# Optimization experiments

Measured on AMD Instinct MI355X. Metric: run time of the kernel, lower is better.

## Reference

```python
import jax, jax.numpy as jnp
import numpy as np

S, B = 1000, 64
E, P, D, O = 512, 256, 1024, 128  # embedding_dim, prenet_dim, decoder_dim, output_dim


def setup_inputs() -> dict:
    key = jax.random.key(0)
    ks = jax.random.split(key, 12)
    u = lambda k, shape: jax.random.uniform(k, shape, jnp.float32, -0.1, 0.1)
    return {
        "encoder_out": jax.random.normal(ks[0], (S, B, E), jnp.float32),
        "mels": jax.random.normal(ks[1], (S, B, O), jnp.float32),
        # prenet layer 0: Linear(O -> P), layer 1: Linear(P -> P)
        "pre_W1": u(ks[2], (P, O)), "pre_b1": u(ks[3], (P,)),
        "pre_W2": u(ks[4], (P, P)), "pre_b2": u(ks[5], (P,)),
        # LSTMCell(input=P+E, hidden=D); gate order i,f,g,o
        "W_ih": u(ks[6], (4 * D, P + E)), "W_hh": u(ks[7], (4 * D, D)),
        "b_ih": u(ks[8], (4 * D,)), "b_hh": u(ks[9], (4 * D,)),
        # projection: Linear(D+E -> O)
        "proj_W": u(ks[10], (O, D + E)), "proj_b": u(ks[11], (O,)),
    }


def reference(encoder_out, mels, pre_W1, pre_b1, pre_W2, pre_b2,
              W_ih, W_hh, b_ih, b_hh, proj_W, proj_b):
    # Teacher forcing: prepend <GO> zero frame, drop last mel frame (only S inputs used)
    go = jnp.zeros((1, B, O), encoder_out.dtype)
    dec_in = jnp.concatenate([go, mels[:-1]], axis=0)  # [S, B, O]
    # Prenet (dropout in eval mode => identity), vectorized over all frames
    x = jax.nn.relu(jnp.einsum('sbo,po->sbp', dec_in, pre_W1) + pre_b1)
    x = jax.nn.relu(jnp.einsum('sbp,qp->sbq', x, pre_W2) + pre_b2)  # [S, B, P]
    # Pre-compute input-to-hidden gate contributions for every frame (big GEMM once)
    lstm_in = jnp.concatenate([x, encoder_out], axis=-1)  # [S, B, P+E]
    gates_x = jnp.einsum('sbi,gi->sbg', lstm_in, W_ih) + b_ih + b_hh  # [S, B, 4D]

    def step(carry, gx_t):
        h, c = carry
        gates = gx_t + h @ W_hh.T  # [B, 4D]
        i, f, g, o = jnp.split(gates, 4, axis=-1)
        c_new = jax.nn.sigmoid(f) * c + jax.nn.sigmoid(i) * jnp.tanh(g)
        h_new = jax.nn.sigmoid(o) * jnp.tanh(c_new)
        # zoneout=0.0 -> new state kept exactly
        return (h_new, c_new), h_new

    h0 = jnp.zeros((B, D), encoder_out.dtype)
    c0 = jnp.zeros((B, D), encoder_out.dtype)
    _, hs = jax.lax.scan(step, (h0, c0), gates_x)  # hs: [S, B, D]

    out = jnp.concatenate([hs, encoder_out], axis=-1)  # [S, B, D+E]
    return jnp.einsum('sbd,od->sbo', out, proj_W) + proj_b  # [S, B, O]
```

## Files before the change

kernel.cpp:

```cpp
#include <hip/hip_runtime.h>
#include <stdint.h>

typedef __bf16 bf16x8 __attribute__((ext_vector_type(8)));
typedef float f32x4 __attribute__((ext_vector_type(4)));
typedef unsigned short ushort_t;

__device__ __forceinline__ float b2f(ushort_t u) {
  union { unsigned int i; float f; } x; x.i = ((unsigned int)u) << 16; return x.f;
}
__device__ __forceinline__ ushort_t f2b(float f) {
  union { float f; unsigned int i; } x; x.f = f;
  unsigned int r = x.i + 0x7fffu + ((x.i >> 16) & 1u);
  return (ushort_t)(r >> 16);
}
__device__ __forceinline__ float b2f_elem(ushort4 v, int j) {
  const ushort_t u = (j == 0) ? v.x : (j == 1) ? v.y : (j == 2) ? v.z : v.w;
  return b2f(u);
}
__device__ __forceinline__ float ftanh(float x) {
  const float e2 = __expf(2.f * x);
  return 1.f - 2.f / (e2 + 1.f);
}

__global__ __launch_bounds__(256) void cvt_f32_bf16(const float* __restrict__ src,
                                                    ushort_t* __restrict__ dst,
                                                    int n4)
{
  const int i = blockIdx.x * 256 + threadIdx.x;
  if (i >= n4) return;
  const float4 v = ((const float4*)src)[i];
  ushort4 o;
  o.x = f2b(v.x); o.y = f2b(v.y); o.z = f2b(v.z); o.w = f2b(v.w);
  ((ushort4*)dst)[i] = o;
}

__global__ __launch_bounds__(256) void build_decin(const float* __restrict__ mels,
                                                   ushort_t* __restrict__ dec,
                                                   int t0, int n4)
{
  const int i = blockIdx.x * 256 + threadIdx.x;
  if (i >= n4) return;
  const int gr = t0 * 64 + (i >> 5);
  ushort4 o;
  if (gr < 64) {
    o.x = o.y = o.z = o.w = 0;
  } else {
    const float4 v = ((const float4*)mels)[(size_t)(gr - 64) * 32 + (i & 31)];
    o.x = f2b(v.x); o.y = f2b(v.y); o.z = f2b(v.z); o.w = f2b(v.w);
  }
  ((ushort4*)dec)[i] = o;
}

__global__ __launch_bounds__(256) void gemm_bt(
    const ushort_t* __restrict__ A1, int lda1, int K1,
    const ushort_t* __restrict__ A2, int lda2, int K2,
    const ushort_t* __restrict__ B,
    const float* __restrict__ bias1, const float* __restrict__ bias2,
    void* __restrict__ C, int ldc, int relu, int out_f32)
{
  __shared__ __align__(16) ushort_t As[128 * 72];
  __shared__ __align__(16) ushort_t Bs[128 * 72];
  const int tid = threadIdx.x;
  const int wave = tid >> 6, lane = tid & 63;
  const int bm = blockIdx.x, bn = blockIdx.y;
  const int wm = (wave & 1) * 64, wn = (wave >> 1) * 64;
  const int l15 = lane & 15, quad = lane >> 4;
  const int ldb = K1 + K2;

  f32x4 acc[4][4] = {};

  const int kb1 = K1 >> 6, kb2 = K2 >> 6;
  for (int kb = 0; kb < kb1 + kb2; ++kb) {
    const bool ph2 = (kb >= kb1);
    const ushort_t* Aptr = ph2 ? A2 : A1;
    const int lda = ph2 ? lda2 : lda1;
    const int k0 = ph2 ? ((kb - kb1) << 6) : (kb << 6);
    const int bk0 = ph2 ? (K1 + k0) : k0;

#pragma unroll
    for (int s = 0; s < 4; ++s) {
      const int ch = s * 256 + tid;
      const int row = ch >> 3, pos = ch & 7;
      const bf16x8 av = *(const bf16x8*)(Aptr + (size_t)(bm * 128 + row) * lda
                                         + k0 + pos * 8);
      *(bf16x8*)(As + row * 72 + pos * 8) = av;
      const bf16x8 bv = *(const bf16x8*)(B + (size_t)(bn * 128 + row) * ldb
                                         + bk0 + pos * 8);
      *(bf16x8*)(Bs + row * 72 + pos * 8) = bv;
    }
    __syncthreads();

#pragma unroll
    for (int ks = 0; ks < 2; ++ks) {
      bf16x8 af[4], bfr[4];
      const int c = ks * 4 + quad;
#pragma unroll
      for (int mt = 0; mt < 4; ++mt)
        af[mt] = *(const bf16x8*)(As + (wm + mt * 16 + l15) * 72 + c * 8);
#pragma unroll
      for (int nt = 0; nt < 4; ++nt)
        bfr[nt] = *(const bf16x8*)(Bs + (wn + nt * 16 + l15) * 72 + c * 8);
#pragma unroll
      for (int mt = 0; mt < 4; ++mt)
#pragma unroll
        for (int nt = 0; nt < 4; ++nt)
          acc[mt][nt] = __builtin_amdgcn_mfma_f32_16x16x32_bf16(
              af[mt], bfr[nt], acc[mt][nt], 0, 0, 0);
    }
    __syncthreads();
  }

#pragma unroll
  for (int nt = 0; nt < 4; ++nt) {
    const int n = bn * 128 + wn + nt * 16 + l15;
    float bsum = 0.f;
    if (bias1) bsum += bias1[n];
    if (bias2) bsum += bias2[n];
#pragma unroll
    for (int mt = 0; mt < 4; ++mt) {
#pragma unroll
      for (int r = 0; r < 4; ++r) {
        const int m = bm * 128 + wm + mt * 16 + quad * 4 + r;
        float v = acc[mt][nt][r] + bsum;
        if (relu) v = fmaxf(v, 0.f);
        if (out_f32) ((float*)C)[(size_t)m * ldc + n] = v;
        else         ((ushort_t*)C)[(size_t)m * ldc + n] = f2b(v);
      }
    }
  }
}

__global__ __launch_bounds__(256, 1) void lstm_persist(
    const ushort_t* __restrict__ gates,
    const ushort_t* __restrict__ Whh,
    ushort_t* __restrict__ hs,
    float* __restrict__ cst,
    int T, int* __restrict__ flags,
    int expect)
{
  __shared__ float red[4][2][64][17];
  const int tid = threadIdx.x;
  const int g = tid >> 6, lane = tid & 63;
  const int l15 = lane & 15, quad = lane >> 4;
  const int nb = blockIdx.x;
  const int ds = nb * 16;

  bf16x8 warr[4][8];
#pragma unroll
  for (int gg = 0; gg < 4; ++gg) {
    const ushort_t* wrow =
        Whh + (size_t)(gg * 1024 + ds + l15) * 1024 + g * 256 + quad * 8;
#pragma unroll
    for (int ks = 0; ks < 8; ++ks)
      warr[gg][ks] = *(const bf16x8*)(wrow + ks * 32);
  }

  const int eb = tid >> 2, edl = (tid & 3) * 4;
  f32x4 creg = *(const f32x4*)(cst + eb * 1024 + ds + edl);

  for (int s = 0; s < T; ++s) {
    const ushort_t* gx_t =
        gates + (size_t)s * 262144 + (size_t)eb * 4096 + ds + edl;
    const ushort4 gxv0 = *(const ushort4*)(gx_t);
    const ushort4 gxv1 = *(const ushort4*)(gx_t + 1024);
    const ushort4 gxv2 = *(const ushort4*)(gx_t + 2048);
    const ushort4 gxv3 = *(const ushort4*)(gx_t + 3072);
    asm volatile("" ::: "memory");

    if (s > 0) {
      int* fp = flags + (s - 1) * 64 + lane;
      int v = __hip_atomic_load(fp, __ATOMIC_RELAXED, __HIP_MEMORY_SCOPE_AGENT);
      while (!__all(v == expect)) {
        __builtin_amdgcn_s_sleep(1);
        v = __hip_atomic_load(fp, __ATOMIC_RELAXED, __HIP_MEMORY_SCOPE_AGENT);
      }
      asm volatile("" ::: "memory");
    }

    const ushort_t* hb =
        hs + (size_t)s * 65536 + l15 * 1024 + g * 256 + quad * 8;
    f32x4 acc[4][4] = {};
#pragma unroll
    for (int ks = 0; ks < 8; ++ks) {
      bf16x8 a[4];
#pragma unroll
      for (int mt = 0; mt < 4; ++mt)
        a[mt] = *(const bf16x8*)(hb + mt * 16384 + ks * 32);
#pragma unroll
      for (int gg = 0; gg < 4; ++gg)
#pragma unroll
        for (int mt = 0; mt < 4; ++mt)
          acc[gg][mt] = __builtin_amdgcn_mfma_f32_16x16x32_bf16(
              a[mt], warr[gg][ks], acc[gg][mt], 0, 0, 0);
    }

    float gf4[4][4];
#pragma unroll
    for (int rnd = 0; rnd < 2; ++rnd) {
#pragma unroll
      for (int ggl = 0; ggl < 2; ++ggl) {
        const int gg = rnd * 2 + ggl;
#pragma unroll
        for (int mt = 0; mt < 4; ++mt)
#pragma unroll
          for (int r = 0; r < 4; ++r)
            red[g][ggl][mt * 16 + quad * 4 + r][l15] = acc[gg][mt][r];
      }
      __syncthreads();
#pragma unroll
      for (int ggl = 0; ggl < 2; ++ggl)
#pragma unroll
        for (int j = 0; j < 4; ++j)
          gf4[rnd * 2 + ggl][j] =
              red[0][ggl][eb][edl + j] + red[1][ggl][eb][edl + j] +
              red[2][ggl][eb][edl + j] + red[3][ggl][eb][edl + j];
      if (rnd == 0) __syncthreads();
    }

    ushort_t* hdst = hs + (size_t)(s + 1) * 65536 + eb * 1024 + ds + edl;
    union { ushort_t u[4]; unsigned long long ll; } pk;
#pragma unroll
    for (int j = 0; j < 4; ++j) {
      const float gi = gf4[0][j] + b2f_elem(gxv0, j);
      const float gf = gf4[1][j] + b2f_elem(gxv1, j);
      const float gc = gf4[2][j] + b2f_elem(gxv2, j);
      const float go = gf4[3][j] + b2f_elem(gxv3, j);
      const float si = 1.f / (1.f + __expf(-gi));
      const float sf = 1.f / (1.f + __expf(-gf));
      const float so = 1.f / (1.f + __expf(-go));
      const float cn = sf * creg[j] + si * ftanh(gc);
      creg[j] = cn;
      pk.u[j] = f2b(so * ftanh(cn));
    }
    __hip_atomic_store((unsigned long long*)hdst, pk.ll,
                       __ATOMIC_RELAXED, __HIP_MEMORY_SCOPE_AGENT);

    __syncthreads();
    if (tid == 0)
      __hip_atomic_store(flags + s * 64 + nb, expect,
                         __ATOMIC_RELAXED, __HIP_MEMORY_SCOPE_AGENT);
  }

  *(f32x4*)(cst + eb * 1024 + ds + edl) = creg;
}

extern "C" void kernel_launch(void* const* d_in, const int* in_sizes, int n_in,
                              void* d_out, int out_size, void* d_ws, size_t ws_size,
                              hipStream_t stream) {
  const float* enc   = (const float*)d_in[0];
  const float* mels  = (const float*)d_in[1];
  const float* preW1 = (const float*)d_in[2];
  const float* preb1 = (const float*)d_in[3];
  const float* preW2 = (const float*)d_in[4];
  const float* preb2 = (const float*)d_in[5];
  const float* Wih   = (const float*)d_in[6];
  const float* Whh   = (const float*)d_in[7];
  const float* bih   = (const float*)d_in[8];
  const float* bhh   = (const float*)d_in[9];
  const float* projW = (const float*)d_in[10];
  const float* projb = (const float*)d_in[11];
  float* out = (float*)d_out;

  const size_t fixedB = 32768 * 2 + 65536 * 2 + 3145728 * 2 + 4194304 * 2
                      + 196608 * 2 + 262144 + 51456 + 65536;
  const int cand[5] = {200, 100, 50, 10, 2};
  int T = 2;
  for (int ci = 0; ci < 5; ++ci) {
    const int t = cand[ci];
    size_t need = fixedB
                + (size_t)t * 524288
                + (size_t)t * 16384
                + (size_t)t * 65536
                + (size_t)t * 32768 * 2
                + (size_t)(t + 1) * 131072;
    if (need <= ws_size) { T = t; break; }
  }

  char* ws = (char*)d_ws;
  size_t off = 0;
  auto carve = [&](size_t bytes) {
    char* p = ws + off;
    off += (bytes + 255) & ~(size_t)255;
    return p;
  };
  ushort_t* wW1  = (ushort_t*)carve(32768 * 2);
  ushort_t* wW2  = (ushort_t*)carve(65536 * 2);
  ushort_t* wIh  = (ushort_t*)carve(3145728 * 2);
  ushort_t* wHh  = (ushort_t*)carve(4194304 * 2);
  ushort_t* wPj  = (ushort_t*)carve(196608 * 2);
  float*    cst  = (float*)carve(262144);
  int*      flags = (int*)carve(51200);
  ushort_t* gates = (ushort_t*)carve((size_t)T * 524288);
  ushort_t* decin = (ushort_t*)carve((size_t)T * 16384);
  ushort_t* enc_c = (ushort_t*)carve((size_t)T * 65536);
  ushort_t* x1    = (ushort_t*)carve((size_t)T * 32768);
  ushort_t* x2    = (ushort_t*)carve((size_t)T * 32768);
  ushort_t* hs    = (ushort_t*)carve((size_t)(T + 1) * 131072);

  cvt_f32_bf16<<<32, 256, 0, stream>>>(preW1, wW1, 8192);
  cvt_f32_bf16<<<64, 256, 0, stream>>>(preW2, wW2, 16384);
  cvt_f32_bf16<<<3072, 256, 0, stream>>>(Wih, wIh, 786432);
  cvt_f32_bf16<<<4096, 256, 0, stream>>>(Whh, wHh, 1048576);
  cvt_f32_bf16<<<192, 256, 0, stream>>>(projW, wPj, 49152);

  hipMemsetAsync(hs, 0, 131072, stream);
  hipMemsetAsync(cst, 0, 262144, stream);
  hipMemsetAsync(flags, 0, 51200, stream);

  const int nch = 1000 / T;
  const int Mb = (T * 64) / 128;

  for (int c = 0; c < nch; ++c) {
    const int t0 = c * T;

    cvt_f32_bf16<<<(T * 8192 + 255) / 256, 256, 0, stream>>>(
        enc + (size_t)t0 * 32768, enc_c, T * 8192);
    build_decin<<<T * 8, 256, 0, stream>>>(mels, decin, t0, T * 2048);

    gemm_bt<<<dim3(Mb, 2), 256, 0, stream>>>(decin, 128, 128, nullptr, 0, 0,
                                             wW1, preb1, nullptr, x1, 256, 1, 0);
    gemm_bt<<<dim3(Mb, 2), 256, 0, stream>>>(x1, 256, 256, nullptr, 0, 0,
                                             wW2, preb2, nullptr, x2, 256, 1, 0);
    gemm_bt<<<dim3(Mb, 32), 256, 0, stream>>>(x2, 256, 256, enc_c, 512, 512,
                                              wIh, bih, bhh, gates, 4096, 0, 0);
    lstm_persist<<<64, 256, 0, stream>>>(gates, wHh, hs, cst, T, flags, c + 1);

    gemm_bt<<<dim3(Mb, 1), 256, 0, stream>>>(hs + 65536, 1024, 1024, enc_c,
                                             512, 512, wPj, projb, nullptr,
                                             out + (size_t)t0 * 8192, 128, 0, 1);
    if (c + 1 < nch) {
      hipMemcpyAsync(hs, hs + (size_t)T * 65536, 131072,
                     hipMemcpyDeviceToDevice, stream);
    }
  }
}
```

Baseline: 8.337 ms.

## Stage h via global_load_lds into swizzled LDS and use per-wave flags

Each wave now copies its K-slice of the previous hidden state from global memory into a swizzled LDS buffer using direct global-to-LDS loads, then reads the MFMA A operands from LDS instead of issuing scattered global loads. Step completion flags go from one per block to one per wave, so a wave waits only on the 64 producer waves that wrote the K-slice it reads, not on whole blocks, and the block-wide barrier before signalling is removed. This aims to shorten the per-step latency of the serial recurrence. In exchange it adds a larger LDS footprint, an extra barrier, a fourfold larger flag array, and more flag polling traffic.

```diff
diff --git a/kernel.cpp b/kernel.cpp
--- a/kernel.cpp
+++ b/kernel.cpp
@@ -138,7 +138,10 @@
     int T, int* __restrict__ flags,
     int expect)
 {
-  __shared__ float red[4][2][64][17];
+  __shared__ __align__(16) ushort_t hq[4 * 64 * 256];
+  float* red = (float*)hq;
+#define RED(w, ggl, row, col) red[(((w) * 2 + (ggl)) * 64 + (row)) * 17 + (col)]
+
   const int tid = threadIdx.x;
   const int g = tid >> 6, lane = tid & 63;
   const int l15 = lane & 15, quad = lane >> 4;
@@ -157,6 +160,11 @@
 
   const int eb = tid >> 2, edl = (tid & 3) * 4;
   f32x4 creg = *(const f32x4*)(cst + eb * 1024 + ds + edl);
+
+  const int l5 = lane >> 5;
+  const int gc = lane & 31;
+  const int sx = l15 & 7;
+  ushort_t* hqg = hq + g * 16384;
 
   for (int s = 0; s < T; ++s) {
     const ushort_t* gx_t =
@@ -168,7 +176,7 @@
     asm volatile("" ::: "memory");
 
     if (s > 0) {
-      int* fp = flags + (s - 1) * 64 + lane;
+      int* fp = flags + (s - 1) * 256 + g * 64 + lane;
       int v = __hip_atomic_load(fp, __ATOMIC_RELAXED, __HIP_MEMORY_SCOPE_AGENT);
       while (!__all(v == expect)) {
         __builtin_amdgcn_s_sleep(1);
@@ -177,15 +185,29 @@
       asm volatile("" ::: "memory");
     }
 
-    const ushort_t* hb =
-        hs + (size_t)s * 65536 + l15 * 1024 + g * 256 + quad * 8;
+    {
+      const ushort_t* hsrc = hs + (size_t)s * 65536;
+#pragma unroll
+      for (int i = 0; i < 32; ++i) {
+        const int row = 2 * i + l5;
+        const int sg = gc ^ (row & 7);
+        const ushort_t* ga = hsrc + (size_t)row * 1024 + g * 256 + sg * 8;
+        __builtin_amdgcn_global_load_lds(
+            (const __attribute__((address_space(1))) void*)ga,
+            (__attribute__((address_space(3))) void*)(hqg + i * 512),
+            16, 0, 0);
+      }
+    }
+    asm volatile("s_waitcnt vmcnt(0)" ::: "memory");
+
     f32x4 acc[4][4] = {};
 #pragma unroll
     for (int ks = 0; ks < 8; ++ks) {
+      const int c = ks * 4 + quad;
       bf16x8 a[4];
 #pragma unroll
       for (int mt = 0; mt < 4; ++mt)
-        a[mt] = *(const bf16x8*)(hb + mt * 16384 + ks * 32);
+        a[mt] = *(const bf16x8*)(hqg + (mt * 16 + l15) * 256 + (c ^ sx) * 8);
 #pragma unroll
       for (int gg = 0; gg < 4; ++gg)
 #pragma unroll
@@ -193,6 +215,7 @@
           acc[gg][mt] = __builtin_amdgcn_mfma_f32_16x16x32_bf16(
               a[mt], warr[gg][ks], acc[gg][mt], 0, 0, 0);
     }
+    __syncthreads();
 
     float gf4[4][4];
 #pragma unroll
@@ -204,7 +227,7 @@
         for (int mt = 0; mt < 4; ++mt)
 #pragma unroll
           for (int r = 0; r < 4; ++r)
-            red[g][ggl][mt * 16 + quad * 4 + r][l15] = acc[gg][mt][r];
+            RED(g, ggl, mt * 16 + quad * 4 + r, l15) = acc[gg][mt][r];
       }
       __syncthreads();
 #pragma unroll
@@ -212,8 +235,8 @@
 #pragma unroll
         for (int j = 0; j < 4; ++j)
           gf4[rnd * 2 + ggl][j] =
-              red[0][ggl][eb][edl + j] + red[1][ggl][eb][edl + j] +
-              red[2][ggl][eb][edl + j] + red[3][ggl][eb][edl + j];
+              RED(0, ggl, eb, edl + j) + RED(1, ggl, eb, edl + j) +
+              RED(2, ggl, eb, edl + j) + RED(3, ggl, eb, edl + j);
       if (rnd == 0) __syncthreads();
     }
 
@@ -223,25 +246,27 @@
     for (int j = 0; j < 4; ++j) {
       const float gi = gf4[0][j] + b2f_elem(gxv0, j);
       const float gf = gf4[1][j] + b2f_elem(gxv1, j);
-      const float gc = gf4[2][j] + b2f_elem(gxv2, j);
+      const float gc_ = gf4[2][j] + b2f_elem(gxv2, j);
       const float go = gf4[3][j] + b2f_elem(gxv3, j);
       const float si = 1.f / (1.f + __expf(-gi));
       const float sf = 1.f / (1.f + __expf(-gf));
       const float so = 1.f / (1.f + __expf(-go));
-      const float cn = sf * creg[j] + si * ftanh(gc);
+      const float cn = sf * creg[j] + si * ftanh(gc_);
       creg[j] = cn;
       pk.u[j] = f2b(so * ftanh(cn));
     }
     __hip_atomic_store((unsigned long long*)hdst, pk.ll,
                        __ATOMIC_RELAXED, __HIP_MEMORY_SCOPE_AGENT);
 
+    asm volatile("s_waitcnt vmcnt(0)" ::: "memory");
+    if (lane == 0)
+      __hip_atomic_store(flags + s * 256 + nb * 4 + g, expect,
+                         __ATOMIC_RELAXED, __HIP_MEMORY_SCOPE_AGENT);
     __syncthreads();
-    if (tid == 0)
-      __hip_atomic_store(flags + s * 64 + nb, expect,
-                         __ATOMIC_RELAXED, __HIP_MEMORY_SCOPE_AGENT);
   }
 
   *(f32x4*)(cst + eb * 1024 + ds + edl) = creg;
+#undef RED
 }
 
 extern "C" void kernel_launch(void* const* d_in, const int* in_sizes, int n_in,
@@ -262,7 +287,7 @@
   float* out = (float*)d_out;
 
   const size_t fixedB = 32768 * 2 + 65536 * 2 + 3145728 * 2 + 4194304 * 2
-                      + 196608 * 2 + 262144 + 51456 + 65536;
+                      + 196608 * 2 + 262144 + 204800 + 65536;
   const int cand[5] = {200, 100, 50, 10, 2};
   int T = 2;
   for (int ci = 0; ci < 5; ++ci) {
@@ -289,7 +314,7 @@
   ushort_t* wHh  = (ushort_t*)carve(4194304 * 2);
   ushort_t* wPj  = (ushort_t*)carve(196608 * 2);
   float*    cst  = (float*)carve(262144);
-  int*      flags = (int*)carve(51200);
+  int*      flags = (int*)carve(204800);
   ushort_t* gates = (ushort_t*)carve((size_t)T * 524288);
   ushort_t* decin = (ushort_t*)carve((size_t)T * 16384);
   ushort_t* enc_c = (ushort_t*)carve((size_t)T * 65536);
@@ -305,7 +330,7 @@
 
   hipMemsetAsync(hs, 0, 131072, stream);
   hipMemsetAsync(cst, 0, 262144, stream);
-  hipMemsetAsync(flags, 0, 51200, stream);
+  hipMemsetAsync(flags, 0, 204800, stream);
 
   const int nch = 1000 / T;
   const int Mb = (T * 64) / 128;
```

New measurement: 6.906 ms. 1.21x faster.

## Use per-wave flags, double-buffered LDS reduction, and hoisted h loads in LSTM

Applied to the files above, without the earlier changes.

Each wave now publishes its own completion flag once its stores drain (s_waitcnt vmcnt(0)), replacing the block-wide barrier before a single flag. The spin-wait drops the sleep and each wave polls 64 flags (256 per step in total). The cross-wave reduction uses a double-buffered LDS array with vectorized f32x4 writes, so it needs one barrier per step instead of three. All h-tile loads are issued before the MFMA chain to overlap memory latency. The costs are more registers, 4x larger flag storage, and busier polling traffic.

```diff
diff --git a/kernel.cpp b/kernel.cpp
--- a/kernel.cpp
+++ b/kernel.cpp
@@ -138,7 +138,8 @@
     int T, int* __restrict__ flags,
     int expect)
 {
-  __shared__ float red[4][2][64][17];
+  __shared__ __align__(16) float red[2][4][4][16][68];
+
   const int tid = threadIdx.x;
   const int g = tid >> 6, lane = tid & 63;
   const int l15 = lane & 15, quad = lane >> 4;
@@ -157,6 +158,8 @@
 
   const int eb = tid >> 2, edl = (tid & 3) * 4;
   f32x4 creg = *(const f32x4*)(cst + eb * 1024 + ds + edl);
+
+  const size_t abase = (size_t)l15 * 1024 + g * 256 + quad * 8;
 
   for (int s = 0; s < T; ++s) {
     const ushort_t* gx_t =
@@ -168,54 +171,45 @@
     asm volatile("" ::: "memory");
 
     if (s > 0) {
-      int* fp = flags + (s - 1) * 64 + lane;
-      int v = __hip_atomic_load(fp, __ATOMIC_RELAXED, __HIP_MEMORY_SCOPE_AGENT);
-      while (!__all(v == expect)) {
-        __builtin_amdgcn_s_sleep(1);
-        v = __hip_atomic_load(fp, __ATOMIC_RELAXED, __HIP_MEMORY_SCOPE_AGENT);
-      }
+      int* fp = flags + (s - 1) * 256 + g * 64 + lane;
+      while (!__all(__hip_atomic_load(fp, __ATOMIC_RELAXED,
+                                      __HIP_MEMORY_SCOPE_AGENT) == expect)) {}
       asm volatile("" ::: "memory");
     }
 
-    const ushort_t* hb =
-        hs + (size_t)s * 65536 + l15 * 1024 + g * 256 + quad * 8;
+    const ushort_t* hsrc = hs + (size_t)s * 65536 + abase;
+    bf16x8 a[8][4];
+#pragma unroll
+    for (int ks = 0; ks < 8; ++ks)
+#pragma unroll
+      for (int mt = 0; mt < 4; ++mt)
+        a[ks][mt] = *(const bf16x8*)(hsrc + (size_t)mt * 16384 + ks * 32);
+
     f32x4 acc[4][4] = {};
 #pragma unroll
-    for (int ks = 0; ks < 8; ++ks) {
-      bf16x8 a[4];
-#pragma unroll
-      for (int mt = 0; mt < 4; ++mt)
-        a[mt] = *(const bf16x8*)(hb + mt * 16384 + ks * 32);
+    for (int ks = 0; ks < 8; ++ks)
 #pragma unroll
       for (int gg = 0; gg < 4; ++gg)
 #pragma unroll
         for (int mt = 0; mt < 4; ++mt)
           acc[gg][mt] = __builtin_amdgcn_mfma_f32_16x16x32_bf16(
-              a[mt], warr[gg][ks], acc[gg][mt], 0, 0, 0);
-    }
+              a[ks][mt], warr[gg][ks], acc[gg][mt], 0, 0, 0);
+
+    auto rb = red[s & 1];
+#pragma unroll
+    for (int gg = 0; gg < 4; ++gg)
+#pragma unroll
+      for (int mt = 0; mt < 4; ++mt)
+        *(f32x4*)&rb[g][gg][l15][mt * 16 + quad * 4] = acc[gg][mt];
+    __syncthreads();
 
     float gf4[4][4];
 #pragma unroll
-    for (int rnd = 0; rnd < 2; ++rnd) {
-#pragma unroll
-      for (int ggl = 0; ggl < 2; ++ggl) {
-        const int gg = rnd * 2 + ggl;
-#pragma unroll
-        for (int mt = 0; mt < 4; ++mt)
-#pragma unroll
-          for (int r = 0; r < 4; ++r)
-            red[g][ggl][mt * 16 + quad * 4 + r][l15] = acc[gg][mt][r];
-      }
-      __syncthreads();
-#pragma unroll
-      for (int ggl = 0; ggl < 2; ++ggl)
-#pragma unroll
-        for (int j = 0; j < 4; ++j)
-          gf4[rnd * 2 + ggl][j] =
-              red[0][ggl][eb][edl + j] + red[1][ggl][eb][edl + j] +
-              red[2][ggl][eb][edl + j] + red[3][ggl][eb][edl + j];
-      if (rnd == 0) __syncthreads();
-    }
+    for (int gg = 0; gg < 4; ++gg)
+#pragma unroll
+      for (int j = 0; j < 4; ++j)
+        gf4[gg][j] = rb[0][gg][edl + j][eb] + rb[1][gg][edl + j][eb] +
+                     rb[2][gg][edl + j][eb] + rb[3][gg][edl + j][eb];
 
     ushort_t* hdst = hs + (size_t)(s + 1) * 65536 + eb * 1024 + ds + edl;
     union { ushort_t u[4]; unsigned long long ll; } pk;
@@ -223,21 +217,21 @@
     for (int j = 0; j < 4; ++j) {
       const float gi = gf4[0][j] + b2f_elem(gxv0, j);
       const float gf = gf4[1][j] + b2f_elem(gxv1, j);
-      const float gc = gf4[2][j] + b2f_elem(gxv2, j);
+      const float gc_ = gf4[2][j] + b2f_elem(gxv2, j);
       const float go = gf4[3][j] + b2f_elem(gxv3, j);
       const float si = 1.f / (1.f + __expf(-gi));
       const float sf = 1.f / (1.f + __expf(-gf));
       const float so = 1.f / (1.f + __expf(-go));
-      const float cn = sf * creg[j] + si * ftanh(gc);
+      const float cn = sf * creg[j] + si * ftanh(gc_);
       creg[j] = cn;
       pk.u[j] = f2b(so * ftanh(cn));
     }
     __hip_atomic_store((unsigned long long*)hdst, pk.ll,
                        __ATOMIC_RELAXED, __HIP_MEMORY_SCOPE_AGENT);
 
-    __syncthreads();
-    if (tid == 0)
-      __hip_atomic_store(flags + s * 64 + nb, expect,
+    asm volatile("s_waitcnt vmcnt(0)" ::: "memory");
+    if (lane == 0)
+      __hip_atomic_store(flags + s * 256 + nb * 4 + g, expect,
                          __ATOMIC_RELAXED, __HIP_MEMORY_SCOPE_AGENT);
   }
 
@@ -262,7 +256,7 @@
   float* out = (float*)d_out;
 
   const size_t fixedB = 32768 * 2 + 65536 * 2 + 3145728 * 2 + 4194304 * 2
-                      + 196608 * 2 + 262144 + 51456 + 65536;
+                      + 196608 * 2 + 262144 + 204800 + 65536;
   const int cand[5] = {200, 100, 50, 10, 2};
   int T = 2;
   for (int ci = 0; ci < 5; ++ci) {
@@ -289,7 +283,7 @@
   ushort_t* wHh  = (ushort_t*)carve(4194304 * 2);
   ushort_t* wPj  = (ushort_t*)carve(196608 * 2);
   float*    cst  = (float*)carve(262144);
-  int*      flags = (int*)carve(51200);
+  int*      flags = (int*)carve(204800);
   ushort_t* gates = (ushort_t*)carve((size_t)T * 524288);
   ushort_t* decin = (ushort_t*)carve((size_t)T * 16384);
   ushort_t* enc_c = (ushort_t*)carve((size_t)T * 65536);
@@ -305,7 +299,7 @@
 
   hipMemsetAsync(hs, 0, 131072, stream);
   hipMemsetAsync(cst, 0, 262144, stream);
-  hipMemsetAsync(flags, 0, 51200, stream);
+  hipMemsetAsync(flags, 0, 204800, stream);
 
   const int nch = 1000 / T;
   const int Mb = (T * 64) / 128;
```

After: 8.906 ms. 1.07x slower.
